# Kernel optimization log

Hardware: AMD Instinct MI355X
Metric: run time of the kernel (lower is better)

## Reference

```python
import jax, jax.numpy as jnp
import numpy as np

N = 500_000   # total nodes in batched graph
E = 10_000_000  # total edges
G = 1_000     # number of graphs in the batch
H = 8         # hidden_dim
C = 8         # n_classes


def setup_inputs() -> dict:
    key = jax.random.key(0)
    k1, k2, k3, k4, k5, k6 = jax.random.split(key, 6)
    src = jax.random.randint(k1, (E,), 0, N)
    dst = jax.random.randint(k2, (E,), 0, N)
    graph_ids = jnp.sort(jax.random.randint(k3, (N,), 0, G))
    W1 = jax.random.normal(k4, (1, H), dtype=jnp.float32) * 0.5
    W2 = jax.random.normal(k5, (H, H), dtype=jnp.float32) * 0.3
    Wlast = jax.random.normal(k6, (H, C), dtype=jnp.float32) * 0.3
    return {"W1": W1, "W2": W2, "Wlast": Wlast,
            "src": src, "dst": dst, "graph_ids": graph_ids}


def reference(W1, W2, Wlast, src, dst, graph_ids):
    ones_e = jnp.ones(src.shape[0], dtype=jnp.float32)
    deg_in = jax.ops.segment_sum(ones_e, dst, num_segments=N)   # in-degrees
    deg_out = jax.ops.segment_sum(ones_e, src, num_segments=N)  # out-degrees
    # DGL GraphConv norm='both': clamp degrees to >=1, then pow(-1/2)
    inv_sqrt_out = jnp.maximum(deg_out, 1.0) ** -0.5
    inv_sqrt_in = jnp.maximum(deg_in, 1.0) ** -0.5

    def gconv(h, W):
        # h: [N, d]; gather-scatter message passing, then dense transform
        h = h * inv_sqrt_out[:, None]
        agg = jax.ops.segment_sum(h[src], dst, num_segments=N)
        return (agg * inv_sqrt_in[:, None]) @ W

    h = deg_in[:, None]  # input feature = in_degrees, shape [N, 1]
    h = jax.nn.relu(gconv(h, W1))
    h = jax.nn.relu(gconv(h, W2))

    # dgl.mean_nodes: per-graph mean over nodes
    counts = jax.ops.segment_sum(jnp.ones(N, dtype=jnp.float32), graph_ids,
                                 num_segments=G)
    hg = jax.ops.segment_sum(h, graph_ids, num_segments=G)
    hg = hg / jnp.maximum(counts, 1.0)[:, None]
    return hg @ Wlast  # [G, n_classes], Linear with bias=False
```

## Files before the change

kernel.cpp:

```cpp
#include <hip/hip_runtime.h>


#define TB 256
#define DTB 512
#define STB 512
#define BSH 13
#define BNODES 8192
#define MAXNB 64
#define SCH 4096
#define SCH4 (SCH / 4)
#define EPT 8
#define CSTR 16
#define INVB 0xFFFFFFFFu

typedef __attribute__((ext_vector_type(4))) int int4v;
typedef __attribute__((ext_vector_type(4))) unsigned uint4v;
typedef __attribute__((ext_vector_type(2))) unsigned uint2v;
typedef __attribute__((ext_vector_type(4))) float float4v;

__global__ void init_kernel(unsigned* __restrict__ curD, unsigned* __restrict__ curS,
                            float* __restrict__ Xsum, int NB, unsigned CAP, int G) {
    int i = blockIdx.x * TB + threadIdx.x;
    if (i < NB) { curD[i * CSTR] = (unsigned)i * CAP; curS[i * CSTR] = (unsigned)i * CAP; }
    if (i < G) Xsum[i] = 0.0f;
}

__global__ void scatter_sort_kernel(const int* __restrict__ src, const int* __restrict__ dst,
                                    unsigned* __restrict__ curD, unsigned* __restrict__ curS,
                                    unsigned* __restrict__ dstP, unsigned short* __restrict__ srcP,
                                    int NB, int E, int blk0) {
    __shared__ unsigned cntD[MAXNB], cntS[MAXNB];
    __shared__ unsigned deltaD[MAXNB], deltaS[MAXNB];
    __shared__ unsigned totD_s, totS_s;
    __shared__ unsigned payD[SCH];
    __shared__ unsigned short valS[SCH];
    __shared__ unsigned char mapD[SCH], mapS[SCH];

    int tid = threadIdx.x;
    if (tid < MAXNB) { cntD[tid] = 0u; cntS[tid] = 0u; }
    __syncthreads();

    unsigned sA[EPT], dA[EPT], bD[EPT], bS[EPT];
    int blk = blockIdx.x + blk0;
#pragma unroll
    for (int v = 0; v < 2; ++v) {
        int q = blk * SCH4 + v * STB + tid;
        int be = q * 4;
        if (be + 3 < E) {
            int4v s4 = __builtin_nontemporal_load((const int4v*)src + q);
            int4v d4 = __builtin_nontemporal_load((const int4v*)dst + q);
#pragma unroll
            for (int k = 0; k < 4; ++k) {
                sA[v*4+k] = (unsigned)s4[k];
                dA[v*4+k] = (unsigned)d4[k];
                bD[v*4+k] = dA[v*4+k] >> BSH;
                bS[v*4+k] = sA[v*4+k] >> BSH;
            }
        } else {
#pragma unroll
            for (int k = 0; k < 4; ++k) {
                int j = be + k;
                if (j < E) {
                    sA[v*4+k] = (unsigned)src[j];
                    dA[v*4+k] = (unsigned)dst[j];
                    bD[v*4+k] = dA[v*4+k] >> BSH;
                    bS[v*4+k] = sA[v*4+k] >> BSH;
                } else {
                    bD[v*4+k] = INVB; bS[v*4+k] = INVB;
                    sA[v*4+k] = 0u; dA[v*4+k] = 0u;
                }
            }
        }
    }

#pragma unroll
    for (int k = 0; k < EPT; ++k) {
        if (bD[k] != INVB) {
            atomicAdd(&cntD[bD[k]], 1u);
            atomicAdd(&cntS[bS[k]], 1u);
        }
    }
    __syncthreads();

    int wv = tid >> 6, ln = tid & 63;
    if (wv == 0) {
        unsigned x = (ln < NB) ? cntD[ln] : 0u;
        unsigned inc = x;
#pragma unroll
        for (int o = 1; o < 64; o <<= 1) {
            unsigned y = __shfl_up(inc, o, 64);
            if (ln >= o) inc += y;
        }
        unsigned exc = inc - x;
        if (ln < NB) {
            unsigned gb = atomicAdd(&curD[ln * CSTR], x);
            deltaD[ln] = gb - exc;
            cntD[ln] = exc;
        }
        if (ln == 63) totD_s = inc;
    } else if (wv == 1) {
        unsigned x = (ln < NB) ? cntS[ln] : 0u;
        unsigned inc = x;
#pragma unroll
        for (int o = 1; o < 64; o <<= 1) {
            unsigned y = __shfl_up(inc, o, 64);
            if (ln >= o) inc += y;
        }
        unsigned exc = inc - x;
        if (ln < NB) {
            unsigned gb = atomicAdd(&curS[ln * CSTR], x);
            deltaS[ln] = gb - exc;
            cntS[ln] = exc;
        }
        if (ln == 63) totS_s = inc;
    }
    __syncthreads();

#pragma unroll
    for (int k = 0; k < EPT; ++k) {
        if (bD[k] != INVB) {
            unsigned p = atomicAdd(&cntD[bD[k]], 1u);
            payD[p] = ((dA[k] & (BNODES - 1)) << 19) | sA[k];
            mapD[p] = (unsigned char)bD[k];
            unsigned p2 = atomicAdd(&cntS[bS[k]], 1u);
            valS[p2] = (unsigned short)(sA[k] & (BNODES - 1));
            mapS[p2] = (unsigned char)bS[k];
        }
    }
    __syncthreads();

    unsigned tD = totD_s, tS = totS_s;
    for (unsigned i = tid; i < tD; i += STB) {
        unsigned b = mapD[i];
        dstP[deltaD[b] + i] = payD[i];
    }
    for (unsigned i = tid; i < tS; i += STB) {
        unsigned b = mapS[i];
        srcP[deltaS[b] + i] = valS[i];
    }
}

__global__ void deghist_kernel(const unsigned short* __restrict__ srcP, const unsigned* __restrict__ dstP,
                               const unsigned* __restrict__ curS, const unsigned* __restrict__ curD,
                               unsigned CAP, unsigned* __restrict__ pDeg, int Jlg) {
    __shared__ unsigned h[BNODES];
    {
        uint4v* hv = (uint4v*)h;
        for (int t = threadIdx.x; t < BNODES / 4; t += DTB) hv[t] = (uint4v)0u;
    }
    __syncthreads();
    int b = blockIdx.x >> Jlg;
    int j = blockIdx.x & ((1 << Jlg) - 1);
    unsigned s0 = (unsigned)b * CAP;

    {
        unsigned cD = curD[b * CSTR] - s0;
        unsigned lo = (unsigned)(((unsigned long long)cD * (unsigned)j) >> Jlg);
        unsigned hi = (unsigned)(((unsigned long long)cD * (unsigned)(j + 1)) >> Jlg);
        unsigned i0 = (lo + 3u) & ~3u;
        unsigned i1 = hi & ~3u;
        if (i0 >= i1) {
            for (unsigned i = lo + threadIdx.x; i < hi; i += DTB)
                atomicAdd(&h[dstP[s0 + i] >> 19], 0x10000u);
        } else {
            if (threadIdx.x < i0 - lo)
                atomicAdd(&h[dstP[s0 + lo + threadIdx.x] >> 19], 0x10000u);
            const uint4v* qp = (const uint4v*)(dstP + s0);
            for (unsigned q = i0 / 4u + threadIdx.x; q < i1 / 4u; q += DTB) {
                uint4v e4 = qp[q];
                atomicAdd(&h[e4.x >> 19], 0x10000u);
                atomicAdd(&h[e4.y >> 19], 0x10000u);
                atomicAdd(&h[e4.z >> 19], 0x10000u);
                atomicAdd(&h[e4.w >> 19], 0x10000u);
            }
            if (threadIdx.x < hi - i1)
                atomicAdd(&h[dstP[s0 + i1 + threadIdx.x] >> 19], 0x10000u);
        }
    }
    {
        unsigned cS = curS[b * CSTR] - s0;
        unsigned lo = (unsigned)(((unsigned long long)cS * (unsigned)j) >> Jlg);
        unsigned hi = (unsigned)(((unsigned long long)cS * (unsigned)(j + 1)) >> Jlg);
        unsigned i0 = (lo + 3u) & ~3u;
        unsigned i1 = hi & ~3u;
        if (i0 >= i1) {
            for (unsigned i = lo + threadIdx.x; i < hi; i += DTB)
                atomicAdd(&h[__builtin_nontemporal_load(&srcP[s0 + i])], 1u);
        } else {
            if (threadIdx.x < i0 - lo)
                atomicAdd(&h[srcP[s0 + lo + threadIdx.x]], 1u);
            const uint2v* qp = (const uint2v*)(srcP + s0);
            for (unsigned q = i0 / 4u + threadIdx.x; q < i1 / 4u; q += DTB) {
                uint2v e2 = __builtin_nontemporal_load(qp + q);
                atomicAdd(&h[e2.x & 0xFFFFu], 1u);
                atomicAdd(&h[e2.x >> 16], 1u);
                atomicAdd(&h[e2.y & 0xFFFFu], 1u);
                atomicAdd(&h[e2.y >> 16], 1u);
            }
            if (threadIdx.x < hi - i1)
                atomicAdd(&h[srcP[s0 + i1 + threadIdx.x]], 1u);
        }
    }
    __syncthreads();
    uint4v* rowv = (uint4v*)(pDeg + (size_t)blockIdx.x * BNODES);
    uint4v* hv = (uint4v*)h;
    for (int t = threadIdx.x; t < BNODES / 4; t += DTB) rowv[t] = hv[t];
}

__global__ void prep_kernel(const unsigned* __restrict__ pDeg,
                            float* __restrict__ pio, float* __restrict__ h0s,
                            float* __restrict__ isiA, int Jlg, int Npad) {
    int i = blockIdx.x * TB + threadIdx.x;
    if (i >= Npad) return;
    int b = i >> BSH, l = i & (BNODES - 1);
    int J = 1 << Jlg;
    unsigned sum = 0;
    for (int j = 0; j < J; ++j)
        sum += __builtin_nontemporal_load(&pDeg[(size_t)((b << Jlg) + j) * BNODES + l]);
    float din = (float)(sum >> 16), dout = (float)(sum & 0xFFFFu);
    float a  = 1.0f / sqrtf(fmaxf(din, 1.0f));
    float bo = 1.0f / sqrtf(fmaxf(dout, 1.0f));
    pio[i]  = a * bo;
    h0s[i]  = din * bo;
    isiA[i] = a;
}

template <int LAST>
__global__ void wh_kernel(const unsigned* __restrict__ dstP, const unsigned* __restrict__ curD,
                          unsigned CAP, const float* __restrict__ table,
                          float* __restrict__ pOut, int Jlg) {
    __shared__ float h[BNODES];
    {
        float4v* hv = (float4v*)h;
        for (int t = threadIdx.x; t < BNODES / 4; t += DTB) hv[t] = (float4v)0.0f;
    }
    __syncthreads();
    int b = blockIdx.x >> Jlg;
    int j = blockIdx.x & ((1 << Jlg) - 1);
    unsigned s0 = (unsigned)b * CAP;
    unsigned cD = curD[b * CSTR] - s0;
    unsigned lo = (unsigned)(((unsigned long long)cD * (unsigned)j) >> Jlg);
    unsigned hi = (unsigned)(((unsigned long long)cD * (unsigned)(j + 1)) >> Jlg);
    unsigned i0 = (lo + 3u) & ~3u;
    unsigned i1 = hi & ~3u;
    if (i0 >= i1) {
        for (unsigned i = lo + threadIdx.x; i < hi; i += DTB) {
            unsigned e = dstP[s0 + i];
            atomicAdd(&h[e >> 19], table[e & 0x7FFFFu]);
        }
    } else {
        if (threadIdx.x < i0 - lo) {
            unsigned e = dstP[s0 + lo + threadIdx.x];
            atomicAdd(&h[e >> 19], table[e & 0x7FFFFu]);
        }
        const uint4v* qp = (const uint4v*)(dstP + s0);
        for (unsigned q = i0 / 4u + threadIdx.x; q < i1 / 4u; q += DTB) {
            uint4v e4 = LAST ? __builtin_nontemporal_load(qp + q) : qp[q];
            float t0 = table[e4.x & 0x7FFFFu];
            float t1 = table[e4.y & 0x7FFFFu];
            float t2 = table[e4.z & 0x7FFFFu];
            float t3 = table[e4.w & 0x7FFFFu];
            atomicAdd(&h[e4.x >> 19], t0);
            atomicAdd(&h[e4.y >> 19], t1);
            atomicAdd(&h[e4.z >> 19], t2);
            atomicAdd(&h[e4.w >> 19], t3);
        }
        if (threadIdx.x < hi - i1) {
            unsigned e = dstP[s0 + i1 + threadIdx.x];
            atomicAdd(&h[e >> 19], table[e & 0x7FFFFu]);
        }
    }
    __syncthreads();
    float4v* rowv = (float4v*)(pOut + (size_t)blockIdx.x * BNODES);
    float4v* hv = (float4v*)h;
    for (int t = threadIdx.x; t < BNODES / 4; t += DTB) rowv[t] = hv[t];
}

__global__ void mid_kernel(const float* __restrict__ pC, const float* __restrict__ pio,
                           float* __restrict__ sarr, int Jlg, int Npad) {
    int i = blockIdx.x * TB + threadIdx.x;
    if (i >= Npad) return;
    int b = i >> BSH, l = i & (BNODES - 1);
    int J = 1 << Jlg;
    float t1 = 0.0f;
    for (int j = 0; j < J; ++j)
        t1 += __builtin_nontemporal_load(&pC[(size_t)((b << Jlg) + j) * BNODES + l]);
    sarr[i] = t1 * pio[i];
}

__global__ void poolfinal_kernel(const float* __restrict__ pT, const float* __restrict__ isiA,
                                 const int* __restrict__ graph_ids,
                                 float* __restrict__ Xsum, int Jlg, int N) {
    int i = blockIdx.x * TB + threadIdx.x;
    bool valid = i < N;
    int ii = valid ? i : (N - 1);
    int b = ii >> BSH, l = ii & (BNODES - 1);
    int J = 1 << Jlg;
    float t2 = 0.0f;
    for (int j = 0; j < J; ++j)
        t2 += __builtin_nontemporal_load(&pT[(size_t)((b << Jlg) + j) * BNODES + l]);
    float x = valid ? t2 * isiA[ii] : 0.0f;
    int g = graph_ids[ii];
    int g0 = __shfl(g, 0, 64);
    bool uniform = __all((!valid) || (g == g0));
    if (uniform) {
#pragma unroll
        for (int off = 32; off >= 1; off >>= 1) x += __shfl_down(x, off, 64);
        if ((threadIdx.x & 63) == 0) atomicAdd(&Xsum[g0], x);
    } else if (valid) {
        atomicAdd(&Xsum[g], x);
    }
}

__global__ void final_kernel(const float* __restrict__ Xsum, const int* __restrict__ graph_ids,
                             const float* __restrict__ W1, const float* __restrict__ W2,
                             const float* __restrict__ Wlast,
                             float* __restrict__ out, int N, int GC) {
    int i = blockIdx.x * TB + threadIdx.x;
    if (i < GC) {
        int g = i >> 3, j = i & 7;
        int lo = 0, hi = N;
        while (lo < hi) { int m = (lo + hi) >> 1; if (graph_ids[m] < g) lo = m + 1; else hi = m; }
        int lo2 = lo, hi2 = N;
        while (lo2 < hi2) { int m = (lo2 + hi2) >> 1; if (graph_ids[m] < g + 1) lo2 = m + 1; else hi2 = m; }
        float c = (float)(lo2 - lo);
        float r = 0.0f;
#pragma unroll
        for (int cc = 0; cc < 8; ++cc) {
            float m = 0.0f;
#pragma unroll
            for (int k = 0; k < 8; ++k) m += fmaxf(W1[k], 0.0f) * W2[k * 8 + cc];
            r += fmaxf(m, 0.0f) * Wlast[cc * 8 + j];
        }
        out[i] = Xsum[g] / fmaxf(c, 1.0f) * r;
    }
}


__global__ void fb_deg_kernel(const int* __restrict__ src, const int* __restrict__ dst,
                              float* __restrict__ deg_out, float* __restrict__ deg_in, int E) {
    int i = blockIdx.x * TB + threadIdx.x;
    if (i < E) {
        atomicAdd(&deg_out[src[i]], 1.0f);
        atomicAdd(&deg_in[dst[i]], 1.0f);
    }
}

__global__ void fb_prep_kernel(const float* __restrict__ deg_in, const float* __restrict__ deg_out,
                               float* __restrict__ isi, float* __restrict__ iso,
                               float* __restrict__ h0s, int N) {
    int i = blockIdx.x * TB + threadIdx.x;
    if (i < N) {
        float di = deg_in[i], dn = deg_out[i];
        float a = 1.0f / sqrtf(fmaxf(di, 1.0f));
        float b = 1.0f / sqrtf(fmaxf(dn, 1.0f));
        isi[i] = a; iso[i] = b; h0s[i] = di * b;
    }
}

__global__ void fb_conv_kernel(const int* __restrict__ src, const int* __restrict__ dst,
                               const float* __restrict__ vals, float* __restrict__ t, int E) {
    int i = blockIdx.x * TB + threadIdx.x;
    if (i < E) atomicAdd(&t[dst[i]], vals[src[i]]);
}

__global__ void fb_mid_kernel(const float* __restrict__ agg1, const float* __restrict__ isi,
                              const float* __restrict__ iso, float* __restrict__ s, int N) {
    int i = blockIdx.x * TB + threadIdx.x;
    if (i < N) s[i] = agg1[i] * isi[i] * iso[i];
}

__global__ void fb_pool_kernel(const float* __restrict__ t2, const float* __restrict__ isi,
                               const int* __restrict__ graph_ids,
                               float* __restrict__ Xsum, float* __restrict__ counts, int N) {
    int i = blockIdx.x * TB + threadIdx.x;
    bool valid = i < N;
    int ii = valid ? i : (N - 1);
    float x = valid ? t2[ii] * isi[ii] : 0.0f;
    float cnt = valid ? 1.0f : 0.0f;
    int g = graph_ids[ii];
    int g0 = __shfl(g, 0, 64);
    bool uniform = __all((!valid) || (g == g0));
    if (uniform) {
#pragma unroll
        for (int off = 32; off >= 1; off >>= 1) {
            x += __shfl_down(x, off, 64);
            cnt += __shfl_down(cnt, off, 64);
        }
        if ((threadIdx.x & 63) == 0) { atomicAdd(&Xsum[g0], x); atomicAdd(&counts[g0], cnt); }
    } else if (valid) {
        atomicAdd(&Xsum[g], x); atomicAdd(&counts[g], 1.0f);
    }
}

__global__ void fb_final_kernel(const float* __restrict__ Xsum, const float* __restrict__ counts,
                                const float* __restrict__ W1, const float* __restrict__ W2,
                                const float* __restrict__ Wlast, float* __restrict__ out, int GC) {
    int i = blockIdx.x * TB + threadIdx.x;
    if (i < GC) {
        int g = i >> 3, j = i & 7;
        float r = 0.0f;
#pragma unroll
        for (int c = 0; c < 8; ++c) {
            float m = 0.0f;
#pragma unroll
            for (int k = 0; k < 8; ++k) m += fmaxf(W1[k], 0.0f) * W2[k * 8 + c];
            r += fmaxf(m, 0.0f) * Wlast[c * 8 + j];
        }
        out[i] = Xsum[g] / fmaxf(counts[g], 1.0f) * r;
    }
}


extern "C" void kernel_launch(void* const* d_in, const int* in_sizes, int n_in,
                              void* d_out, int out_size, void* d_ws, size_t ws_size,
                              hipStream_t stream) {
    const float* W1        = (const float*)d_in[0];
    const float* W2        = (const float*)d_in[1];
    const float* Wlast     = (const float*)d_in[2];
    const int*   src       = (const int*)d_in[3];
    const int*   dst       = (const int*)d_in[4];
    const int*   graph_ids = (const int*)d_in[5];
    float* out = (float*)d_out;

    const int E = in_sizes[3];
    const int N = in_sizes[5];
    const int G = out_size / 8;

    int NB   = (N + BNODES - 1) >> BSH;
    int Npad = NB << BSH;
    int NCH  = (E + SCH - 1) / SCH;
    unsigned CAP = (unsigned)(((E / (NB > 0 ? NB : 1)) + 8192 + 511) & ~511);

    int Jlg = 4;
    size_t req = 0;
    size_t o_dstP, o_srcP, o_curD, o_curS, o_part, o_pio, o_h0sar, o_isi, o_Xsum;
    for (;; --Jlg) {
        int J = 1 << Jlg;
        size_t off = 0;
        auto A = [&](size_t bytes) { size_t o = off; off = (off + bytes + 127) & ~(size_t)127; return o; };
        o_dstP  = A((size_t)NB * CAP * 4);
        o_srcP  = A((size_t)NB * CAP * 2);
        o_curD  = A((size_t)NB * CSTR * 4);
        o_curS  = A((size_t)NB * CSTR * 4);
        o_part  = A((size_t)NB * J * BNODES * 4);
        o_pio   = A((size_t)Npad * 4);
        o_h0sar = A((size_t)Npad * 4);
        o_isi   = A((size_t)Npad * 4);
        o_Xsum  = A((size_t)G * 4);
        req = off;
        if (req <= ws_size || Jlg == 0) break;
    }

    bool fast = (N <= (1 << 19)) && (NB <= MAXNB) && (ws_size >= req) && (E >= 1);

    char* bp = (char*)d_ws;

    if (fast) {
        unsigned*       dstP = (unsigned*)(bp + o_dstP);
        unsigned short* srcP = (unsigned short*)(bp + o_srcP);
        unsigned* curD = (unsigned*)(bp + o_curD);
        unsigned* curS = (unsigned*)(bp + o_curS);
        unsigned* pDeg = (unsigned*)(bp + o_part);
        float*    pC   = (float*)(bp + o_part);
        float*    pT   = (float*)(bp + o_part);
        float* pio  = (float*)(bp + o_pio);
        float* h0s  = (float*)(bp + o_h0sar);
        float* sarr = (float*)(bp + o_h0sar);
        float* isiA = (float*)(bp + o_isi);
        float* Xsum = (float*)(bp + o_Xsum);

        int gridNp = (Npad + TB - 1) / TB;
        int gridN  = (N + TB - 1) / TB;
        int J = 1 << Jlg;
        int gridI = (max(NB, G) + TB - 1) / TB;

        int NCH1 = (NCH + 1) / 2;
        int NCH2 = NCH - NCH1;

        init_kernel<<<gridI, TB, 0, stream>>>(curD, curS, Xsum, NB, CAP, G);
        scatter_sort_kernel<<<NCH1, STB, 0, stream>>>(src, dst, curD, curS, dstP, srcP, NB, E, 0);
        if (NCH2 > 0)
            scatter_sort_kernel<<<NCH2, STB, 0, stream>>>(src, dst, curD, curS, dstP, srcP, NB, E, NCH1);
        deghist_kernel<<<NB * J, DTB, 0, stream>>>(srcP, dstP, curS, curD, CAP, pDeg, Jlg);
        prep_kernel<<<gridNp, TB, 0, stream>>>(pDeg, pio, h0s, isiA, Jlg, Npad);
        wh_kernel<0><<<NB * J, DTB, 0, stream>>>(dstP, curD, CAP, h0s, pC, Jlg);
        mid_kernel<<<gridNp, TB, 0, stream>>>(pC, pio, sarr, Jlg, Npad);
        wh_kernel<1><<<NB * J, DTB, 0, stream>>>(dstP, curD, CAP, sarr, pT, Jlg);
        poolfinal_kernel<<<gridN, TB, 0, stream>>>(pT, isiA, graph_ids, Xsum, Jlg, N);
        final_kernel<<<(out_size + TB - 1) / TB, TB, 0, stream>>>(Xsum, graph_ids,
                                                                  W1, W2, Wlast, out, N, out_size);
    } else {
        float* ws = (float*)d_ws;
        size_t f = 0;
        auto FA = [&](size_t n) { size_t o = f; f += (n + 3) & ~(size_t)3; return o; };
        size_t f_degin  = FA(N);
        size_t f_degout = FA(N);
        size_t f_agg1   = FA(N);
        size_t f_t2     = FA(N);
        size_t f_Xsum   = FA(G);
        size_t f_cnt    = FA(G);
        size_t zf = f;
        size_t f_isi = FA(N);
        size_t f_iso = FA(N);
        size_t f_h0s = FA(N);
        size_t f_s   = FA(N);
        hipMemsetAsync(ws, 0, zf * sizeof(float), stream);
        int gridE = (E + TB - 1) / TB;
        int gridN = (N + TB - 1) / TB;
        int gridO = (out_size + TB - 1) / TB;
        fb_deg_kernel<<<gridE, TB, 0, stream>>>(src, dst, ws + f_degout, ws + f_degin, E);
        fb_prep_kernel<<<gridN, TB, 0, stream>>>(ws + f_degin, ws + f_degout,
                                                 ws + f_isi, ws + f_iso, ws + f_h0s, N);
        fb_conv_kernel<<<gridE, TB, 0, stream>>>(src, dst, ws + f_h0s, ws + f_agg1, E);
        fb_mid_kernel<<<gridN, TB, 0, stream>>>(ws + f_agg1, ws + f_isi, ws + f_iso, ws + f_s, N);
        fb_conv_kernel<<<gridE, TB, 0, stream>>>(src, dst, ws + f_s, ws + f_t2, E);
        fb_pool_kernel<<<gridN, TB, 0, stream>>>(ws + f_t2, ws + f_isi, graph_ids,
                                                 ws + f_Xsum, ws + f_cnt, N);
        fb_final_kernel<<<gridO, TB, 0, stream>>>(ws + f_Xsum, ws + f_cnt, W1, W2, Wlast,
                                                  out, out_size);
    }
}
```

Measured before the change: 368.8 us.

## Add 2D bucketed edge sort so gather tables fit in shared memory

Adds a new fast path that first buckets edges by destination block, then sub-sorts each bucket by source block into a 2D cell grid. The degree histograms and both message-passing passes then read one 8192-node source slice at a time into LDS, so table lookups hit shared memory instead of doing random global gathers. The separate source-sorted copy is dropped and degrees come from the cell grid. The cost is an extra sort pass over all edges and more workspace, and the old path's vectorized deghist loops are simplified to scalar loops.

```diff
diff --git a/kernel.cpp b/kernel.cpp
--- a/kernel.cpp
+++ b/kernel.cpp
@@ -9,8 +9,11 @@
 #define MAXNB 64
 #define SCH 4096
 #define SCH4 (SCH / 4)
+#define SCH2 4096
 #define EPT 8
 #define CSTR 16
+#define GLG 4
+#define GNUM 16
 #define INVB 0xFFFFFFFFu
 
 typedef __attribute__((ext_vector_type(4))) int int4v;
@@ -19,9 +22,12 @@
 typedef __attribute__((ext_vector_type(4))) float float4v;
 
 __global__ void init_kernel(unsigned* __restrict__ curD, unsigned* __restrict__ curS,
-                            float* __restrict__ Xsum, int NB, unsigned CAP, int G) {
-    int i = blockIdx.x * TB + threadIdx.x;
-    if (i < NB) { curD[i * CSTR] = (unsigned)i * CAP; curS[i * CSTR] = (unsigned)i * CAP; }
+                            unsigned* __restrict__ curC, float* __restrict__ Xsum,
+                            int NB, unsigned CAP, int cells, unsigned CAP2, int G) {
+    int i = blockIdx.x * TB + threadIdx.x;
+    if (i < NB) curD[i * CSTR] = (unsigned)i * CAP;
+    if (curS && i < NB) curS[i * CSTR] = (unsigned)i * CAP;
+    if (curC && i < cells) curC[i * CSTR] = (unsigned)i * CAP2;
     if (i < G) Xsum[i] = 0.0f;
 }
 
@@ -77,7 +83,7 @@
     for (int k = 0; k < EPT; ++k) {
         if (bD[k] != INVB) {
             atomicAdd(&cntD[bD[k]], 1u);
-            atomicAdd(&cntS[bS[k]], 1u);
+            if (srcP) atomicAdd(&cntS[bS[k]], 1u);
         }
     }
     __syncthreads();
@@ -98,7 +104,7 @@
             cntD[ln] = exc;
         }
         if (ln == 63) totD_s = inc;
-    } else if (wv == 1) {
+    } else if (wv == 1 && srcP) {
         unsigned x = (ln < NB) ? cntS[ln] : 0u;
         unsigned inc = x;
 #pragma unroll
@@ -122,23 +128,223 @@
             unsigned p = atomicAdd(&cntD[bD[k]], 1u);
             payD[p] = ((dA[k] & (BNODES - 1)) << 19) | sA[k];
             mapD[p] = (unsigned char)bD[k];
-            unsigned p2 = atomicAdd(&cntS[bS[k]], 1u);
-            valS[p2] = (unsigned short)(sA[k] & (BNODES - 1));
-            mapS[p2] = (unsigned char)bS[k];
-        }
-    }
-    __syncthreads();
-
-    unsigned tD = totD_s, tS = totS_s;
+            if (srcP) {
+                unsigned p2 = atomicAdd(&cntS[bS[k]], 1u);
+                valS[p2] = (unsigned short)(sA[k] & (BNODES - 1));
+                mapS[p2] = (unsigned char)bS[k];
+            }
+        }
+    }
+    __syncthreads();
+
+    unsigned tD = totD_s;
     for (unsigned i = tid; i < tD; i += STB) {
         unsigned b = mapD[i];
         dstP[deltaD[b] + i] = payD[i];
     }
-    for (unsigned i = tid; i < tS; i += STB) {
-        unsigned b = mapS[i];
-        srcP[deltaS[b] + i] = valS[i];
-    }
-}
+    if (srcP) {
+        unsigned tS = totS_s;
+        for (unsigned i = tid; i < tS; i += STB) {
+            unsigned b = mapS[i];
+            srcP[deltaS[b] + i] = valS[i];
+        }
+    }
+}
+
+__global__ void subsort_kernel(const unsigned* __restrict__ dstP, const unsigned* __restrict__ curD,
+                               unsigned* __restrict__ curC, unsigned* __restrict__ dstP2,
+                               unsigned CAP, unsigned CAP2, int NB, int MAXCH) {
+    __shared__ unsigned cnt2[MAXNB], delta2[MAXNB];
+    __shared__ unsigned tot_s;
+    __shared__ unsigned pay[SCH2];
+    __shared__ unsigned char map2[SCH2];
+
+    int db = blockIdx.x / MAXCH, c = blockIdx.x % MAXCH;
+    unsigned s = (unsigned)db * CAP + (unsigned)c * SCH2;
+    unsigned e = curD[db * CSTR];
+    if (s >= e) return;
+    unsigned n = e - s; if (n > SCH2) n = SCH2;
+
+    int tid = threadIdx.x;
+    if (tid < MAXNB) cnt2[tid] = 0u;
+    __syncthreads();
+
+    unsigned pl[EPT], bk[EPT];
+#pragma unroll
+    for (int v = 0; v < 2; ++v) {
+        unsigned q = (unsigned)(v * STB + tid);
+        unsigned base = q * 4u;
+        if (base + 3u < n) {
+            uint4v p4 = *((const uint4v*)(dstP + s) + q);
+#pragma unroll
+            for (int k = 0; k < 4; ++k) {
+                pl[v*4+k] = p4[k];
+                bk[v*4+k] = (p4[k] & 0x7FFFFu) >> BSH;
+            }
+        } else {
+#pragma unroll
+            for (int k = 0; k < 4; ++k) {
+                unsigned j = base + (unsigned)k;
+                if (j < n) {
+                    pl[v*4+k] = dstP[s + j];
+                    bk[v*4+k] = (pl[v*4+k] & 0x7FFFFu) >> BSH;
+                } else { bk[v*4+k] = INVB; pl[v*4+k] = 0u; }
+            }
+        }
+    }
+
+#pragma unroll
+    for (int k = 0; k < EPT; ++k)
+        if (bk[k] != INVB) atomicAdd(&cnt2[bk[k]], 1u);
+    __syncthreads();
+
+    if (tid < 64) {
+        int ln = tid;
+        unsigned x = cnt2[ln];
+        unsigned inc = x;
+#pragma unroll
+        for (int o = 1; o < 64; o <<= 1) {
+            unsigned y = __shfl_up(inc, o, 64);
+            if (ln >= o) inc += y;
+        }
+        unsigned exc = inc - x;
+        if (ln < NB) {
+            unsigned gb = atomicAdd(&curC[((unsigned)db * NB + ln) * CSTR], x);
+            delta2[ln] = gb - exc;
+            cnt2[ln] = exc;
+        }
+        if (ln == 63) tot_s = inc;
+    }
+    __syncthreads();
+
+#pragma unroll
+    for (int k = 0; k < EPT; ++k) {
+        if (bk[k] != INVB) {
+            unsigned p = atomicAdd(&cnt2[bk[k]], 1u);
+            pay[p] = ((pl[k] >> 19) << BSH) | (pl[k] & (BNODES - 1));
+            map2[p] = (unsigned char)bk[k];
+        }
+    }
+    __syncthreads();
+
+    unsigned tot = tot_s;
+    for (unsigned i = tid; i < tot; i += STB) {
+        unsigned b = map2[i];
+        dstP2[delta2[b] + i] = pay[i];
+    }
+}
+
+__global__ void degin2_kernel(const unsigned* __restrict__ dstP2, const unsigned* __restrict__ curC,
+                              unsigned CAP2, unsigned short* __restrict__ pDegIn, int NB, int GS) {
+    __shared__ unsigned h[BNODES];
+    {
+        uint4v* hv = (uint4v*)h;
+        for (int t = threadIdx.x; t < BNODES / 4; t += DTB) hv[t] = (uint4v)0u;
+    }
+    __syncthreads();
+    int db = blockIdx.x >> GLG, g = blockIdx.x & (GNUM - 1);
+    int sbEnd = (g + 1) * GS; if (sbEnd > NB) sbEnd = NB;
+    for (int sb = g * GS; sb < sbEnd; ++sb) {
+        unsigned cell = (unsigned)(db * NB + sb);
+        unsigned lo = cell * CAP2;
+        unsigned hi = curC[cell * CSTR];
+        for (unsigned i = lo + threadIdx.x; i < hi; i += DTB)
+            atomicAdd(&h[dstP2[i] >> BSH], 1u);
+    }
+    __syncthreads();
+    unsigned short* row = pDegIn + (size_t)blockIdx.x * BNODES;
+    for (int t = threadIdx.x; t < BNODES; t += DTB) row[t] = (unsigned short)h[t];
+}
+
+__global__ void degout2_kernel(const unsigned* __restrict__ dstP2, const unsigned* __restrict__ curC,
+                               unsigned CAP2, unsigned short* __restrict__ pDegOut, int NB, int GS) {
+    __shared__ unsigned h[BNODES];
+    {
+        uint4v* hv = (uint4v*)h;
+        for (int t = threadIdx.x; t < BNODES / 4; t += DTB) hv[t] = (uint4v)0u;
+    }
+    __syncthreads();
+    int sb = blockIdx.x >> GLG, g = blockIdx.x & (GNUM - 1);
+    int dbEnd = (g + 1) * GS; if (dbEnd > NB) dbEnd = NB;
+    for (int db = g * GS; db < dbEnd; ++db) {
+        unsigned cell = (unsigned)(db * NB + sb);
+        unsigned lo = cell * CAP2;
+        unsigned hi = curC[cell * CSTR];
+        for (unsigned i = lo + threadIdx.x; i < hi; i += DTB)
+            atomicAdd(&h[dstP2[i] & (BNODES - 1)], 1u);
+    }
+    __syncthreads();
+    unsigned short* row = pDegOut + (size_t)blockIdx.x * BNODES;
+    for (int t = threadIdx.x; t < BNODES; t += DTB) row[t] = (unsigned short)h[t];
+}
+
+__global__ void prep2_kernel(const unsigned short* __restrict__ pDegIn,
+                             const unsigned short* __restrict__ pDegOut,
+                             float* __restrict__ pio, float* __restrict__ h0s,
+                             float* __restrict__ isiA, int Npad) {
+    int i = blockIdx.x * TB + threadIdx.x;
+    if (i >= Npad) return;
+    int b = i >> BSH, l = i & (BNODES - 1);
+    unsigned din_u = 0, dout_u = 0;
+    for (int g = 0; g < GNUM; ++g) {
+        din_u  += __builtin_nontemporal_load(&pDegIn [(size_t)(b * GNUM + g) * BNODES + l]);
+        dout_u += __builtin_nontemporal_load(&pDegOut[(size_t)(b * GNUM + g) * BNODES + l]);
+    }
+    float din = (float)din_u, dout = (float)dout_u;
+    float a  = 1.0f / sqrtf(fmaxf(din, 1.0f));
+    float bo = 1.0f / sqrtf(fmaxf(dout, 1.0f));
+    pio[i]  = a * bo;
+    h0s[i]  = din * bo;
+    isiA[i] = a;
+}
+
+template <int LAST>
+__global__ void wh2d_kernel(const unsigned* __restrict__ dstP2, const unsigned* __restrict__ curC,
+                            unsigned CAP2, const float* __restrict__ table,
+                            float* __restrict__ pOut, int NB, int GS) {
+    __shared__ float h[BNODES];
+    __shared__ float slice[BNODES];
+    {
+        float4v* hv = (float4v*)h;
+        for (int t = threadIdx.x; t < BNODES / 4; t += DTB) hv[t] = (float4v)0.0f;
+    }
+    int db = blockIdx.x >> GLG, g = blockIdx.x & (GNUM - 1);
+    int sbEnd = (g + 1) * GS; if (sbEnd > NB) sbEnd = NB;
+    for (int sb = g * GS; sb < sbEnd; ++sb) {
+        __syncthreads();
+        {
+            const float4v* tp = (const float4v*)(table + ((size_t)sb << BSH));
+            float4v* sp = (float4v*)slice;
+            for (int t = threadIdx.x; t < BNODES / 4; t += DTB) sp[t] = tp[t];
+        }
+        __syncthreads();
+        unsigned cell = (unsigned)(db * NB + sb);
+        unsigned lo = cell * CAP2;
+        unsigned hi = curC[cell * CSTR];
+        unsigned i1 = hi & ~3u;
+        const uint4v* qp = (const uint4v*)(dstP2 + lo);
+        for (unsigned q = threadIdx.x; q < (i1 - lo) / 4u; q += DTB) {
+            uint4v e4 = LAST ? __builtin_nontemporal_load(qp + q) : qp[q];
+            float t0 = slice[e4.x & (BNODES - 1)];
+            float t1 = slice[e4.y & (BNODES - 1)];
+            float t2 = slice[e4.z & (BNODES - 1)];
+            float t3 = slice[e4.w & (BNODES - 1)];
+            atomicAdd(&h[e4.x >> BSH], t0);
+            atomicAdd(&h[e4.y >> BSH], t1);
+            atomicAdd(&h[e4.z >> BSH], t2);
+            atomicAdd(&h[e4.w >> BSH], t3);
+        }
+        if (threadIdx.x < hi - i1) {
+            unsigned e = dstP2[i1 + threadIdx.x];
+            atomicAdd(&h[e >> BSH], slice[e & (BNODES - 1)]);
+        }
+    }
+    __syncthreads();
+    float4v* rowv = (float4v*)(pOut + (size_t)blockIdx.x * BNODES);
+    float4v* hv = (float4v*)h;
+    for (int t = threadIdx.x; t < BNODES / 4; t += DTB) rowv[t] = hv[t];
+}
+
 
 __global__ void deghist_kernel(const unsigned short* __restrict__ srcP, const unsigned* __restrict__ dstP,
                                const unsigned* __restrict__ curS, const unsigned* __restrict__ curD,
@@ -152,54 +358,19 @@
     int b = blockIdx.x >> Jlg;
     int j = blockIdx.x & ((1 << Jlg) - 1);
     unsigned s0 = (unsigned)b * CAP;
-
     {
         unsigned cD = curD[b * CSTR] - s0;
         unsigned lo = (unsigned)(((unsigned long long)cD * (unsigned)j) >> Jlg);
         unsigned hi = (unsigned)(((unsigned long long)cD * (unsigned)(j + 1)) >> Jlg);
-        unsigned i0 = (lo + 3u) & ~3u;
-        unsigned i1 = hi & ~3u;
-        if (i0 >= i1) {
-            for (unsigned i = lo + threadIdx.x; i < hi; i += DTB)
-                atomicAdd(&h[dstP[s0 + i] >> 19], 0x10000u);
-        } else {
-            if (threadIdx.x < i0 - lo)
-                atomicAdd(&h[dstP[s0 + lo + threadIdx.x] >> 19], 0x10000u);
-            const uint4v* qp = (const uint4v*)(dstP + s0);
-            for (unsigned q = i0 / 4u + threadIdx.x; q < i1 / 4u; q += DTB) {
-                uint4v e4 = qp[q];
-                atomicAdd(&h[e4.x >> 19], 0x10000u);
-                atomicAdd(&h[e4.y >> 19], 0x10000u);
-                atomicAdd(&h[e4.z >> 19], 0x10000u);
-                atomicAdd(&h[e4.w >> 19], 0x10000u);
-            }
-            if (threadIdx.x < hi - i1)
-                atomicAdd(&h[dstP[s0 + i1 + threadIdx.x] >> 19], 0x10000u);
-        }
+        for (unsigned i = lo + threadIdx.x; i < hi; i += DTB)
+            atomicAdd(&h[dstP[s0 + i] >> 19], 0x10000u);
     }
     {
         unsigned cS = curS[b * CSTR] - s0;
         unsigned lo = (unsigned)(((unsigned long long)cS * (unsigned)j) >> Jlg);
         unsigned hi = (unsigned)(((unsigned long long)cS * (unsigned)(j + 1)) >> Jlg);
-        unsigned i0 = (lo + 3u) & ~3u;
-        unsigned i1 = hi & ~3u;
-        if (i0 >= i1) {
-            for (unsigned i = lo + threadIdx.x; i < hi; i += DTB)
-                atomicAdd(&h[__builtin_nontemporal_load(&srcP[s0 + i])], 1u);
-        } else {
-            if (threadIdx.x < i0 - lo)
-                atomicAdd(&h[srcP[s0 + lo + threadIdx.x]], 1u);
-            const uint2v* qp = (const uint2v*)(srcP + s0);
-            for (unsigned q = i0 / 4u + threadIdx.x; q < i1 / 4u; q += DTB) {
-                uint2v e2 = __builtin_nontemporal_load(qp + q);
-                atomicAdd(&h[e2.x & 0xFFFFu], 1u);
-                atomicAdd(&h[e2.x >> 16], 1u);
-                atomicAdd(&h[e2.y & 0xFFFFu], 1u);
-                atomicAdd(&h[e2.y >> 16], 1u);
-            }
-            if (threadIdx.x < hi - i1)
-                atomicAdd(&h[srcP[s0 + i1 + threadIdx.x]], 1u);
-        }
+        for (unsigned i = lo + threadIdx.x; i < hi; i += DTB)
+            atomicAdd(&h[__builtin_nontemporal_load(&srcP[s0 + i])], 1u);
     }
     __syncthreads();
     uint4v* rowv = (uint4v*)(pDeg + (size_t)blockIdx.x * BNODES);
@@ -276,6 +447,7 @@
     for (int t = threadIdx.x; t < BNODES / 4; t += DTB) rowv[t] = hv[t];
 }
 
+
 __global__ void mid_kernel(const float* __restrict__ pC, const float* __restrict__ pio,
                            float* __restrict__ sarr, int Jlg, int Npad) {
     int i = blockIdx.x * TB + threadIdx.x;
@@ -431,6 +603,70 @@
     int Npad = NB << BSH;
     int NCH  = (E + SCH - 1) / SCH;
     unsigned CAP = (unsigned)(((E / (NB > 0 ? NB : 1)) + 8192 + 511) & ~511);
+    char* bp = (char*)d_ws;
+
+    bool fast2D = false;
+    size_t q_dstP = 0, q_dstP2 = 0, q_curD = 0, q_curC = 0, q_pio = 0, q_h0sar = 0,
+           q_isi = 0, q_Xsum = 0;
+    int cells = NB * NB;
+    unsigned CAP2 = 0;
+    int GS = (NB + GNUM - 1) / GNUM;
+    if (N <= (1 << 19) && NB <= MAXNB && E >= 1) {
+        CAP2 = (unsigned)(((E / (cells > 0 ? cells : 1)) + 768 + 127) & ~127);
+        size_t off = 0;
+        auto A = [&](size_t bytes) { size_t o = off; off = (off + bytes + 127) & ~(size_t)127; return o; };
+        size_t partBytes = (size_t)NB * GNUM * BNODES * 4;
+        size_t dstPBytes = (size_t)NB * CAP * 4;
+        q_dstP  = A(dstPBytes > partBytes ? dstPBytes : partBytes);
+        q_dstP2 = A((size_t)cells * CAP2 * 4 + (size_t)CAP2 * 4);
+        q_curD  = A((size_t)NB * CSTR * 4);
+        q_curC  = A((size_t)cells * CSTR * 4);
+        q_pio   = A((size_t)Npad * 4);
+        q_h0sar = A((size_t)Npad * 4);
+        q_isi   = A((size_t)Npad * 4);
+        q_Xsum  = A((size_t)G * 4);
+        fast2D = (off <= ws_size);
+    }
+
+    if (fast2D) {
+        unsigned* dstP  = (unsigned*)(bp + q_dstP);
+        unsigned* dstP2 = (unsigned*)(bp + q_dstP2);
+        unsigned* curD  = (unsigned*)(bp + q_curD);
+        unsigned* curC  = (unsigned*)(bp + q_curC);
+        unsigned short* pDegIn  = (unsigned short*)(bp + q_dstP);
+        unsigned short* pDegOut = pDegIn + (size_t)NB * GNUM * BNODES;
+        float* pC   = (float*)(bp + q_dstP);
+        float* pT   = (float*)(bp + q_dstP);
+        float* pio  = (float*)(bp + q_pio);
+        float* h0s  = (float*)(bp + q_h0sar);
+        float* sarr = (float*)(bp + q_h0sar);
+        float* isiA = (float*)(bp + q_isi);
+        float* Xsum = (float*)(bp + q_Xsum);
+
+        int gridNp = (Npad + TB - 1) / TB;
+        int gridN  = (N + TB - 1) / TB;
+        int mx = cells > G ? cells : G; if (NB > mx) mx = NB;
+        int gridI  = (mx + TB - 1) / TB;
+        int MAXCH  = (int)((CAP + SCH2 - 1) / SCH2);
+        int NCH1 = (NCH + 1) / 2;
+        int NCH2 = NCH - NCH1;
+
+        init_kernel<<<gridI, TB, 0, stream>>>(curD, nullptr, curC, Xsum, NB, CAP, cells, CAP2, G);
+        scatter_sort_kernel<<<NCH1, STB, 0, stream>>>(src, dst, curD, nullptr, dstP, nullptr, NB, E, 0);
+        if (NCH2 > 0)
+            scatter_sort_kernel<<<NCH2, STB, 0, stream>>>(src, dst, curD, nullptr, dstP, nullptr, NB, E, NCH1);
+        subsort_kernel<<<NB * MAXCH, STB, 0, stream>>>(dstP, curD, curC, dstP2, CAP, CAP2, NB, MAXCH);
+        degin2_kernel<<<NB * GNUM, DTB, 0, stream>>>(dstP2, curC, CAP2, pDegIn, NB, GS);
+        degout2_kernel<<<NB * GNUM, DTB, 0, stream>>>(dstP2, curC, CAP2, pDegOut, NB, GS);
+        prep2_kernel<<<gridNp, TB, 0, stream>>>(pDegIn, pDegOut, pio, h0s, isiA, Npad);
+        wh2d_kernel<0><<<NB * GNUM, DTB, 0, stream>>>(dstP2, curC, CAP2, h0s, pC, NB, GS);
+        mid_kernel<<<gridNp, TB, 0, stream>>>(pC, pio, sarr, GLG, Npad);
+        wh2d_kernel<1><<<NB * GNUM, DTB, 0, stream>>>(dstP2, curC, CAP2, sarr, pT, NB, GS);
+        poolfinal_kernel<<<gridN, TB, 0, stream>>>(pT, isiA, graph_ids, Xsum, GLG, N);
+        final_kernel<<<(out_size + TB - 1) / TB, TB, 0, stream>>>(Xsum, graph_ids,
+                                                                  W1, W2, Wlast, out, N, out_size);
+        return;
+    }
 
     int Jlg = 4;
     size_t req = 0;
@@ -454,8 +690,6 @@
 
     bool fast = (N <= (1 << 19)) && (NB <= MAXNB) && (ws_size >= req) && (E >= 1);
 
-    char* bp = (char*)d_ws;
-
     if (fast) {
         unsigned*       dstP = (unsigned*)(bp + o_dstP);
         unsigned short* srcP = (unsigned short*)(bp + o_srcP);
@@ -473,12 +707,11 @@
         int gridNp = (Npad + TB - 1) / TB;
         int gridN  = (N + TB - 1) / TB;
         int J = 1 << Jlg;
-        int gridI = (max(NB, G) + TB - 1) / TB;
-
+        int gridI = ((NB > G ? NB : G) + TB - 1) / TB;
         int NCH1 = (NCH + 1) / 2;
         int NCH2 = NCH - NCH1;
 
-        init_kernel<<<gridI, TB, 0, stream>>>(curD, curS, Xsum, NB, CAP, G);
+        init_kernel<<<gridI, TB, 0, stream>>>(curD, curS, nullptr, Xsum, NB, CAP, 0, 0, G);
         scatter_sort_kernel<<<NCH1, STB, 0, stream>>>(src, dst, curD, curS, dstP, srcP, NB, E, 0);
         if (NCH2 > 0)
             scatter_sort_kernel<<<NCH2, STB, 0, stream>>>(src, dst, curD, curS, dstP, srcP, NB, E, NCH1);
```

After: 420.4 us. 14.0% more time.
